# Kernel optimization log

Hardware: AMD Instinct MI355X
Metric: run time of the kernel (lower is better)

The kernel has to match this reference:

```python
import jax, jax.numpy as jnp
import numpy as np

B, DIM, DQ, H, W, K = 64, 64, 8, 64, 64, 64


def setup_inputs() -> dict:
    key = jax.random.key(0)
    k1, k2, k3 = jax.random.split(key, 3)
    features = jax.random.normal(k1, (B, DIM, H, W), dtype=jnp.float32)
    query = jax.random.normal(k2, (B, DQ, H, W), dtype=jnp.float32)
    # Ensemble of K 1x1 convs (Conv2d(dim, dim_query, 1, bias=False)) -> [K, DQ, DIM]
    weight = jax.random.normal(k3, (K, DQ, DIM), dtype=jnp.float32) * (1.0 / np.sqrt(DIM))
    return {"features": features, "query": query, "weight": weight}


def reference(features, query, weight):
    # Ensemble of K 1x1 convs: key_values [k, b, dq, h, w]
    key_values = jnp.einsum('bchw,kqc->kbqhw', features, weight)
    b = query.shape[0]
    q_flat = query.reshape(b, -1)                       # [b, D], D = dq*h*w
    kv_flat = key_values.reshape(K, b, -1)              # [k, b, D]
    # torch.cdist(query[b,1,D], kv[b,k,D]) -> euclidean distance [b, k]
    diff = kv_flat - q_flat[None, :, :]                 # [k, b, D]
    distance = jnp.sqrt(jnp.sum(diff * diff, axis=-1)).T  # [b, k]
    codes = jnp.argmax(-distance, axis=-1)              # [b]
    # gather per-batch selected key_values
    sel_key_values = key_values[codes, jnp.arange(b)]   # [b, dq, h, w]
    commit_loss = jnp.mean((sel_key_values - query) ** 2)
    return sel_key_values, codes, commit_loss
```

## Files before the change

kernel.cpp:

```cpp
#include <hip/hip_runtime.h>

#define BQ   64
#define CDIM 64
#define DQN  8
#define HWN  4096
#define KKN  64

typedef float  f32x4  __attribute__((ext_vector_type(4)));
typedef short  short8 __attribute__((ext_vector_type(8)));

__device__ __forceinline__ ushort f2bf(float x) {
  uint u = __float_as_uint(x);
  u += 0x7fffu + ((u >> 16) & 1u);
  return (ushort)(u >> 16);
}
__device__ __forceinline__ float bf2f(ushort h) {
  return __uint_as_float(((uint)h) << 16);
}

__global__ __launch_bounds__(256) void k_gram(const float* __restrict__ feat,
                                              const float* __restrict__ qry,
                                              float* __restrict__ part, int chb) {
  __shared__ ushort ldsH[80 * 128];
  __shared__ ushort ldsL[80 * 128];
  int tid = threadIdx.x;
  int wv = tid >> 6, lane = tid & 63;
  int blk = blockIdx.x;
  int b = blk / chb, cb = blk - b * chb;
  int CH = 4096 / chb;
  int hwBase = cb * CH;
  int nch = 32 / chb;
  const float* fb = feat + (size_t)b * (CDIM * HWN);
  const float* qb = qry + (size_t)b * (DQN * HWN);

  for (int i = tid; i < 8 * 128; i += 256) {
    ldsH[72 * 128 + i] = 0;
    ldsL[72 * 128 + i] = 0;
  }

  int frow = lane & 15;
  int fk = (lane >> 4) * 8;
  f32x4 acc[5] = {};

  for (int ch = 0; ch < nch; ++ch) {
    int hw0 = hwBase + ch * 128;
    #pragma unroll
    for (int it = 0; it < 9; ++it) {
      int idx = it * 256 + tid;
      int r = idx >> 5;
      int g4 = idx & 31;
      const float* src = (r < 64) ? (fb + (size_t)r * HWN + hw0 + g4 * 4)
                                  : (qb + (size_t)(r - 64) * HWN + hw0 + g4 * 4);
      float4 f = *(const float4*)src;
      ushort h0 = f2bf(f.x), h1 = f2bf(f.y), h2 = f2bf(f.z), h3 = f2bf(f.w);
      ushort l0 = f2bf(f.x - bf2f(h0));
      ushort l1 = f2bf(f.y - bf2f(h1));
      ushort l2 = f2bf(f.z - bf2f(h2));
      ushort l3 = f2bf(f.w - bf2f(h3));
      int uoff = r * 128 + ((g4 * 4) ^ ((r & 7) << 3));
      *(ushort4*)(ldsH + uoff) = make_ushort4(h0, h1, h2, h3);
      *(ushort4*)(ldsL + uoff) = make_ushort4(l0, l1, l2, l3);
    }
    __syncthreads();
    #pragma unroll
    for (int ks = 0; ks < 4; ++ks) {
      short8 fh[5], fl[5];
      #pragma unroll
      for (int t = 0; t < 5; ++t) {
        int row = t * 16 + frow;
        int uo = row * 128 + ((ks * 32 + fk) ^ ((row & 7) << 3));
        fh[t] = *(const short8*)(ldsH + uo);
        fl[t] = *(const short8*)(ldsL + uo);
      }
      int brow = wv * 16 + frow;
      int bo = brow * 128 + ((ks * 32 + fk) ^ ((brow & 7) << 3));
      short8 bh = *(const short8*)(ldsH + bo);
      short8 bl = *(const short8*)(ldsL + bo);
      #pragma unroll
      for (int t = 0; t < 5; ++t) {
        acc[t] = __builtin_amdgcn_mfma_f32_16x16x32_bf16(fh[t], bh, acc[t], 0, 0, 0);
        acc[t] = __builtin_amdgcn_mfma_f32_16x16x32_bf16(fh[t], bl, acc[t], 0, 0, 0);
        acc[t] = __builtin_amdgcn_mfma_f32_16x16x32_bf16(fl[t], bh, acc[t], 0, 0, 0);
      }
    }
    __syncthreads();
  }

  float* op = part + (size_t)blk * 4608 + wv * 16 + (lane & 15);
  int r0 = (lane >> 4) * 4;
  #pragma unroll
  for (int t = 0; t < 5; ++t) {
    #pragma unroll
    for (int r = 0; r < 4; ++r) {
      int row = t * 16 + r0 + r;
      if (row < 72) op[row * 64] = acc[t][r];
    }
  }
}

__global__ __launch_bounds__(256) void k_reduce(const float* __restrict__ part,
                                                float* __restrict__ Sarr,
                                                float* __restrict__ Garr, int chb) {
  int g = blockIdx.x * 256 + threadIdx.x;
  int b = g >> 10;
  b = g / 1152;
  int o = (g - b * 1152) * 4;
  f32x4 s = {};
  #pragma unroll 8
  for (int cb = 0; cb < chb; ++cb) {
    f32x4 p = *(const f32x4*)(part + (size_t)(b * chb + cb) * 4608 + o);
    s += p;
  }
  int r = o >> 6, c = o & 63;
  if (r < 64)
    *(f32x4*)(Sarr + b * 4096 + r * 64 + c) = s;
  else
    *(f32x4*)(Garr + b * 512 + (r - 64) * 64 + c) = s;
}

__global__ __launch_bounds__(256) void k_dist(const float* __restrict__ Sarr,
                                              const float* __restrict__ Garr,
                                              const float* __restrict__ wt,
                                              float* __restrict__ dist) {
  __shared__ float wl[4][512];
  int tid = threadIdx.x, wv = tid >> 6, lane = tid & 63;
  int wid = blockIdx.x * 4 + wv;
  int b = wid >> 6, k = wid & 63;
  for (int t = lane; t < 512; t += 64) wl[wv][t] = wt[k * 512 + t];
  __syncthreads();
  const float* Sb = Sarr + b * 4096;
  float v[8] = {};
  #pragma unroll 4
  for (int j = 0; j < 64; ++j) {
    float s = Sb[j * 64 + lane];
    #pragma unroll
    for (int q = 0; q < 8; ++q) v[q] = fmaf(s, wl[wv][q * 64 + j], v[q]);
  }
  double red = 0.0;
  #pragma unroll
  for (int q = 0; q < 8; ++q) {
    float wqi = wl[wv][q * 64 + lane];
    float gqi = Garr[b * 512 + q * 64 + lane];
    red += (double)wqi * ((double)v[q] - 2.0 * (double)gqi);
  }
  #pragma unroll
  for (int off = 32; off; off >>= 1) red += __shfl_xor(red, off);
  if (lane == 0) dist[b * 64 + k] = (float)red;
}

__global__ void k_argmin(const float* __restrict__ dist, int* __restrict__ codes,
                         float* __restrict__ outCodes) {
  int b = blockIdx.x, k = threadIdx.x;
  float d = dist[b * 64 + k];
  int bi = k;
  #pragma unroll
  for (int off = 32; off; off >>= 1) {
    float d2 = __shfl_xor(d, off);
    int i2 = __shfl_xor(bi, off);
    if (d2 < d || (d2 == d && i2 < bi)) { d = d2; bi = i2; }
  }
  if (k == 0) { codes[b] = bi; outCodes[b] = (float)bi; }
}

__global__ __launch_bounds__(256) void k_select(const float* __restrict__ feat,
                                                const float* __restrict__ qry,
                                                const float* __restrict__ wt,
                                                const int* __restrict__ codes,
                                                float* __restrict__ outSel,
                                                float* __restrict__ lossPart) {
  __shared__ float wl[512];
  __shared__ float lred[4];
  int bid = blockIdx.x, tid = threadIdx.x;
  int b = bid >> 2, chunk = bid & 3;
  int code = codes[b];
  wl[tid] = wt[code * 512 + tid];
  wl[tid + 256] = wt[code * 512 + 256 + tid];
  __syncthreads();
  int hw = chunk * 1024 + tid * 4;
  const float* fb = feat + (size_t)b * (CDIM * HWN);
  float4 acc[8] = {};
  #pragma unroll 4
  for (int c = 0; c < 64; ++c) {
    float4 f = *(const float4*)(fb + c * HWN + hw);
    #pragma unroll
    for (int q = 0; q < 8; ++q) {
      float w = wl[q * 64 + c];
      acc[q].x = fmaf(w, f.x, acc[q].x);
      acc[q].y = fmaf(w, f.y, acc[q].y);
      acc[q].z = fmaf(w, f.z, acc[q].z);
      acc[q].w = fmaf(w, f.w, acc[q].w);
    }
  }
  float lsum = 0.f;
  #pragma unroll
  for (int q = 0; q < 8; ++q) {
    size_t off = (size_t)b * 32768 + q * 4096 + hw;
    float4 qv = *(const float4*)(qry + off);
    *(float4*)(outSel + off) = acc[q];
    float dx = acc[q].x - qv.x, dy = acc[q].y - qv.y;
    float dz = acc[q].z - qv.z, dw = acc[q].w - qv.w;
    lsum += dx * dx + dy * dy + dz * dz + dw * dw;
  }
  #pragma unroll
  for (int off = 32; off; off >>= 1) lsum += __shfl_xor(lsum, off);
  if ((tid & 63) == 0) lred[tid >> 6] = lsum;
  __syncthreads();
  if (tid == 0) lossPart[bid] = lred[0] + lred[1] + lred[2] + lred[3];
}

__global__ void k_loss(const float* __restrict__ lossPart, float* __restrict__ outLoss) {
  __shared__ float lred[4];
  int tid = threadIdx.x;
  float s = lossPart[tid];
  #pragma unroll
  for (int off = 32; off; off >>= 1) s += __shfl_xor(s, off);
  if ((tid & 63) == 0) lred[tid >> 6] = s;
  __syncthreads();
  if (tid == 0) outLoss[0] = (lred[0] + lred[1] + lred[2] + lred[3]) * (1.0f / 2097152.0f);
}

extern "C" void kernel_launch(void* const* d_in, const int* in_sizes, int n_in,
                              void* d_out, int out_size, void* d_ws, size_t ws_size,
                              hipStream_t stream) {
  const float* feat = (const float*)d_in[0];
  const float* qry  = (const float*)d_in[1];
  const float* wt   = (const float*)d_in[2];
  float* out = (float*)d_out;
  float* sel      = out;
  float* outCodes = out + 2097152;
  float* outLoss  = out + 2097216;

  int chb = 8;
  while (chb > 1 &&
         ((size_t)64 * chb * 4608 + 64 * 4096 + 64 * 512 + 4096 + 64 + 256) * 4 > ws_size)
    chb >>= 1;
  float* wsf = (float*)d_ws;
  float* part = wsf;
  float* Sarr = part + (size_t)64 * chb * 4608;
  float* Garr = Sarr + 64 * 4096;
  float* dist = Garr + 64 * 512;
  int*   codes = (int*)(dist + 4096);
  float* lossPart = (float*)(codes + 64);

  k_gram<<<64 * chb, 256, 0, stream>>>(feat, qry, part, chb);
  k_reduce<<<(64 * 1152) / 256, 256, 0, stream>>>(part, Sarr, Garr, chb);
  k_dist<<<1024, 256, 0, stream>>>(Sarr, Garr, wt, dist);
  k_argmin<<<64, 64, 0, stream>>>(dist, codes, outCodes);
  k_select<<<256, 256, 0, stream>>>(feat, qry, wt, codes, sel, lossPart);
  k_loss<<<1, 256, 0, stream>>>(lossPart, outLoss);
}
```

Before: 58.02 us.

## Prefetch next gram chunk into registers while MFMAs run on current tile

The gram kernel now issues global loads for the next 128-column chunk into registers before running the MFMA loop on the current LDS tile, then converts and stores them after a barrier. The aim is to hide global memory latency behind compute. It also precomputes per-thread base pointers and swizzled offsets, truncates the high bf16 part instead of rounding, and reuses already-loaded A fragments as the B operand instead of issuing separate LDS reads. The cost is higher register pressure from nine float4 prefetch buffers and an extra barrier per iteration.

```diff
diff --git a/kernel.cpp b/kernel.cpp
--- a/kernel.cpp
+++ b/kernel.cpp
@@ -16,6 +16,19 @@
 }
 __device__ __forceinline__ float bf2f(ushort h) {
   return __uint_as_float(((uint)h) << 16);
+}
+
+__device__ __forceinline__ void cvtStore(ushort* __restrict__ H,
+                                         ushort* __restrict__ L,
+                                         int uoff, float4 f) {
+  ushort4 h = make_ushort4((ushort)(__float_as_uint(f.x) >> 16),
+                           (ushort)(__float_as_uint(f.y) >> 16),
+                           (ushort)(__float_as_uint(f.z) >> 16),
+                           (ushort)(__float_as_uint(f.w) >> 16));
+  ushort4 l = make_ushort4(f2bf(f.x - bf2f(h.x)), f2bf(f.y - bf2f(h.y)),
+                           f2bf(f.z - bf2f(h.z)), f2bf(f.w - bf2f(h.w)));
+  *(ushort4*)(H + uoff) = h;
+  *(ushort4*)(L + uoff) = l;
 }
 
 __global__ __launch_bounds__(256) void k_gram(const float* __restrict__ feat,
@@ -38,30 +51,41 @@
     ldsL[72 * 128 + i] = 0;
   }
 
+  int g4 = tid & 31;
+  int r8 = tid >> 5;
+  const float* base[9];
+  int uoffs[9];
+  #pragma unroll
+  for (int it = 0; it < 9; ++it) {
+    int r = it * 8 + r8;
+    base[it] = ((r < 64) ? (fb + (size_t)r * HWN)
+                         : (qb + (size_t)(r - 64) * HWN)) + g4 * 4;
+    uoffs[it] = r * 128 + ((g4 * 4) ^ ((r & 7) << 3));
+  }
+
   int frow = lane & 15;
   int fk = (lane >> 4) * 8;
   f32x4 acc[5] = {};
 
+  {
+    float4 cur[9];
+    #pragma unroll
+    for (int it = 0; it < 9; ++it)
+      cur[it] = *(const float4*)(base[it] + hwBase);
+    #pragma unroll
+    for (int it = 0; it < 9; ++it) cvtStore(ldsH, ldsL, uoffs[it], cur[it]);
+  }
+  __syncthreads();
+
   for (int ch = 0; ch < nch; ++ch) {
-    int hw0 = hwBase + ch * 128;
-    #pragma unroll
-    for (int it = 0; it < 9; ++it) {
-      int idx = it * 256 + tid;
-      int r = idx >> 5;
-      int g4 = idx & 31;
-      const float* src = (r < 64) ? (fb + (size_t)r * HWN + hw0 + g4 * 4)
-                                  : (qb + (size_t)(r - 64) * HWN + hw0 + g4 * 4);
-      float4 f = *(const float4*)src;
-      ushort h0 = f2bf(f.x), h1 = f2bf(f.y), h2 = f2bf(f.z), h3 = f2bf(f.w);
-      ushort l0 = f2bf(f.x - bf2f(h0));
-      ushort l1 = f2bf(f.y - bf2f(h1));
-      ushort l2 = f2bf(f.z - bf2f(h2));
-      ushort l3 = f2bf(f.w - bf2f(h3));
-      int uoff = r * 128 + ((g4 * 4) ^ ((r & 7) << 3));
-      *(ushort4*)(ldsH + uoff) = make_ushort4(h0, h1, h2, h3);
-      *(ushort4*)(ldsL + uoff) = make_ushort4(l0, l1, l2, l3);
-    }
-    __syncthreads();
+    float4 nxt[9];
+    bool hasNext = (ch + 1 < nch);
+    if (hasNext) {
+      int hw0 = hwBase + (ch + 1) * 128;
+      #pragma unroll
+      for (int it = 0; it < 9; ++it)
+        nxt[it] = *(const float4*)(base[it] + hw0);
+    }
     #pragma unroll
     for (int ks = 0; ks < 4; ++ks) {
       short8 fh[5], fl[5];
@@ -72,10 +96,13 @@
         fh[t] = *(const short8*)(ldsH + uo);
         fl[t] = *(const short8*)(ldsL + uo);
       }
-      int brow = wv * 16 + frow;
-      int bo = brow * 128 + ((ks * 32 + fk) ^ ((brow & 7) << 3));
-      short8 bh = *(const short8*)(ldsH + bo);
-      short8 bl = *(const short8*)(ldsL + bo);
+      short8 bh, bl;
+      switch (wv) {
+        case 0:  bh = fh[0]; bl = fl[0]; break;
+        case 1:  bh = fh[1]; bl = fl[1]; break;
+        case 2:  bh = fh[2]; bl = fl[2]; break;
+        default: bh = fh[3]; bl = fl[3]; break;
+      }
       #pragma unroll
       for (int t = 0; t < 5; ++t) {
         acc[t] = __builtin_amdgcn_mfma_f32_16x16x32_bf16(fh[t], bh, acc[t], 0, 0, 0);
@@ -84,6 +111,11 @@
       }
     }
     __syncthreads();
+    if (hasNext) {
+      #pragma unroll
+      for (int it = 0; it < 9; ++it) cvtStore(ldsH, ldsL, uoffs[it], nxt[it]);
+      __syncthreads();
+    }
   }
 
   float* op = part + (size_t)blk * 4608 + wv * 16 + (lane & 15);
@@ -102,8 +134,7 @@
                                                 float* __restrict__ Sarr,
                                                 float* __restrict__ Garr, int chb) {
   int g = blockIdx.x * 256 + threadIdx.x;
-  int b = g >> 10;
-  b = g / 1152;
+  int b = g / 1152;
   int o = (g - b * 1152) * 4;
   f32x4 s = {};
   #pragma unroll 8
```

Result: slower. 59.77 us (+3.0%).
